# Kernel optimization log

Hardware: AMD Instinct MI355X
Metric: run time of the kernel (lower is better)

The kernel has to match this reference:

```python
import jax, jax.numpy as jnp
import numpy as np

CEP_ORDER = 255          # M
IR_LENGTH = 512          # N
BATCH = 131072
C_SCALE = 0.01           # keep the exponential-ish recurrence numerically tame


def setup_inputs() -> dict:
    key = jax.random.key(0)
    c = jax.random.normal(key, (BATCH, CEP_ORDER + 1), dtype=jnp.float32) * C_SCALE
    return {"c": c}


def _c2mpir(c, ir_length):
    # c: (..., M+1) -> h: (..., N)
    M = c.shape[-1] - 1
    ramp = jnp.arange(1, M + 1, dtype=c.dtype)
    h0 = jnp.exp(c[..., 0])                      # (...,)
    c1 = (c[..., 1:] * ramp)[..., ::-1]          # (..., M), flipped k*c_k
    # rolling buffer holds h[n-M .. n-1]; zeros stand in for negative indices,
    # which reproduces the truncated window h[max(0, n-M):n] of the original.
    buf0 = jnp.zeros_like(c1).at[..., -1].set(h0)
    ns = jnp.arange(1, ir_length, dtype=c.dtype)

    def step(buf, n):
        hn = jnp.einsum('...d,...d->...', buf, c1) / n      # (...,)
        buf = jnp.concatenate([buf[..., 1:], hn[..., None]], axis=-1)
        return buf, hn

    _, hs = jax.lax.scan(step, buf0, ns)         # (N-1, ...)
    h = jnp.concatenate([h0[None], hs], axis=0)  # (N, ...)
    return jnp.moveaxis(h, 0, -1)                # (..., N)


def reference(c):
    return _c2mpir(c, IR_LENGTH)
```

## Files before the change

### kernel.cpp

```cpp
#include <hip/hip_runtime.h>
#include <math.h>


constexpr int ROWS_PER_BLOCK = 32;
constexpr int THREADS = 256;
constexpr int CLEN = 256;
constexpr int NOUT = 512;
constexpr int RHALVES = 264;

typedef float f4 __attribute__((ext_vector_type(4)));
typedef _Float16 half2_t __attribute__((ext_vector_type(2)));

__device__ __forceinline__ float row8_sum(float v) {
  int x;
  x = __builtin_amdgcn_update_dpp(0, __float_as_int(v), 0xB1, 0xF, 0xF, true);
  v += __int_as_float(x);
  x = __builtin_amdgcn_update_dpp(0, __float_as_int(v), 0x4E, 0xF, 0xF, true);
  v += __int_as_float(x);
  x = __builtin_amdgcn_update_dpp(0, __float_as_int(v), 0x141, 0xF, 0xF, true);
  v += __int_as_float(x);
  return v;
}

#define DOTQ(P, wu, ub)                                                \
      { const half2_t q = __builtin_bit_cast(half2_t, (wu));           \
        A0 = __builtin_amdgcn_fdot2(q, P[(ub) + 7], A0, false);        \
        A1 = __builtin_amdgcn_fdot2(q, P[(ub) + 6], A1, false);        \
        A2 = __builtin_amdgcn_fdot2(q, P[(ub) + 5], A2, false);        \
        A3 = __builtin_amdgcn_fdot2(q, P[(ub) + 4], A3, false);        \
        A4 = __builtin_amdgcn_fdot2(q, P[(ub) + 3], A4, false);        \
        A5 = __builtin_amdgcn_fdot2(q, P[(ub) + 2], A5, false);        \
        A6 = __builtin_amdgcn_fdot2(q, P[(ub) + 1], A6, false);        \
        A7 = __builtin_amdgcn_fdot2(q, P[(ub) + 0], A7, false); }

#define ITER_TAIL(Y0EXPR)                                                \
      const float a0 = row8_sum(A0);                                     \
      const float a1 = row8_sum(A1);                                     \
      const float a2 = row8_sum(A2);                                     \
      const float a3 = row8_sum(A3);                                     \
      const float a4 = row8_sum(A4);                                     \
      const float a5 = row8_sum(A5);                                     \
      const float a6 = row8_sum(A6);                                     \
      const float a7 = row8_sum(A7);                                     \
      const int n = it * 8;                                              \
      const f4 ivA = *(const f4*)(&INV[n]);                              \
      const f4 ivB = *(const f4*)(&INV[n + 4]);                          \
      const float y0 = (Y0EXPR);                                         \
      const float y1 = fmaf(kc1, y0, a1) * ivA.y;                        \
      const float y2 = fmaf(kc1, y1, fmaf(kc2, y0, a2)) * ivA.z;         \
      const float y3 = fmaf(kc1, y2, fmaf(kc2, y1,                       \
                          fmaf(kc3, y0, a3))) * ivA.w;                   \
      const float y4 = fmaf(kc1, y3, fmaf(kc2, y2, fmaf(kc3, y1,         \
                          fmaf(kc4, y0, a4)))) * ivB.x;                  \
      const float y5 = fmaf(kc1, y4, fmaf(kc2, y3, fmaf(kc3, y2,         \
                          fmaf(kc4, y1, fmaf(kc5, y0, a5))))) * ivB.y;   \
      const float y6 = fmaf(kc1, y5, fmaf(kc2, y4, fmaf(kc3, y3,         \
                          fmaf(kc4, y2, fmaf(kc5, y1,                    \
                          fmaf(kc6, y0, a6)))))) * ivB.z;                \
      const float y7 = fmaf(kc1, y6, fmaf(kc2, y5, fmaf(kc3, y4,         \
                          fmaf(kc4, y3, fmaf(kc5, y2, fmaf(kc6, y1,      \
                          fmaf(kc7, y0, a7)))))))  * ivB.w;              \
      uint4 wq;                                                          \
      wq.x = __builtin_bit_cast(uint, __builtin_amdgcn_cvt_pkrtz(y0, y1)); \
      wq.y = __builtin_bit_cast(uint, __builtin_amdgcn_cvt_pkrtz(y2, y3)); \
      wq.z = __builtin_bit_cast(uint, __builtin_amdgcn_cvt_pkrtz(y4, y5)); \
      wq.w = __builtin_bit_cast(uint, __builtin_amdgcn_cvt_pkrtz(y6, y7)); \
      qn = wq;                                                           \
      wo = (wo + 16) & 508;                                              \
      if (s == 0) {                                                      \
        *(uint4*)(Hb + wo) = wq;      \
      }                                                                  \
      if ((it & 7) == s) {                                               \
        ys0 = y0; ys1 = y1; ys2 = y2; ys3 = y3;                          \
        ys4 = y4; ys5 = y5; ys6 = y6; ys7 = y7;                          \
      }                                                                  \
      if ((it & 7) == 7) {                                               \
        f4 v0; v0.x = ys0; v0.y = ys1; v0.z = ys2; v0.w = ys3;           \
        f4 v1; v1.x = ys4; v1.y = ys5; v1.z = ys6; v1.w = ys7;           \
        *(f4*)(gp) = v0;                                                 \
        *(f4*)(gp + 4) = v1;                                             \
        gp += 64;                                                        \
      }

__global__ __launch_bounds__(THREADS, 4) void cep2ir_kernel(
    const float* __restrict__ c, float* __restrict__ out, int nrows) {
  __shared__ ushort HF[ROWS_PER_BLOCK][RHALVES];
  __shared__ float INV[NOUT];

  const int tid = threadIdx.x;
  const int lane = tid & 63;
  const int wid = tid >> 6;
  const int s = lane & 7;
  const int rl = (wid << 3) | (lane >> 3);

  for (int i = tid; i < NOUT; i += THREADS)
    INV[i] = (i == 0) ? 0.0f : 1.0f / (float)i;
  uint* hz = (uint*)&HF[0][0];
  for (int i = tid; i < ROWS_PER_BLOCK * RHALVES / 2; i += THREADS)
    hz[i] = 0u;
  __syncthreads();

  const long long row = (long long)blockIdx.x * ROWS_PER_BLOCK + rl;
  if (row < nrows) {
    const float* __restrict__ crow = c + row * (long long)CLEN;

    const float kc1 = crow[1];
    const float kc2 = 2.0f * crow[2];
    const float kc3 = 3.0f * crow[3];
    const float kc4 = 4.0f * crow[4];
    const float kc5 = 5.0f * crow[5];
    const float kc6 = 6.0f * crow[6];
    const float kc7 = 7.0f * crow[7];
    const float h0val = expf(crow[0]);
    const bool is7 = (s == 7);

    char* __restrict__ Hb = (char*)&HF[rl][0];
    int wo = (-16) & 508;
    float* __restrict__ gp = out + row * (long long)NOUT + 8 * s;

    uint4 qn; qn.x = 0u; qn.y = 0u; qn.z = 0u; qn.w = 0u;

    float ys0 = 0.f, ys1 = 0.f, ys2 = 0.f, ys3 = 0.f;
    float ys4 = 0.f, ys5 = 0.f, ys6 = 0.f, ys7 = 0.f;

    {
      const int K1 = 128 - 16 * s;
      half2_t P1[22];
#pragma unroll
      for (int u = 0; u < 22; ++u) {
        const int kx = K1 + 7 - u;
        P1[u] = __builtin_bit_cast(half2_t, __builtin_amdgcn_cvt_pkrtz(
                    (float)kx * crow[kx], (float)(kx - 1) * crow[kx - 1]));
      }

#pragma unroll 2
      for (int it = 0; it < 16; ++it) {
        const int b0 = (16 * it + 256 + 32 * s) & 508;
        const int b1 = (b0 + 16) & 508;
        const uint4 u0 = *(const uint4*)(Hb + b0);
        const uint4 u1r = *(const uint4*)(Hb + b1);
        uint4 u1;
        u1.x = is7 ? qn.x : u1r.x;
        u1.y = is7 ? qn.y : u1r.y;
        u1.z = is7 ? qn.z : u1r.z;
        u1.w = is7 ? qn.w : u1r.w;

        float A0 = 0.f, A1 = 0.f, A2 = 0.f, A3 = 0.f;
        float A4 = 0.f, A5 = 0.f, A6 = 0.f, A7 = 0.f;
        DOTQ(P1, u0.x, 0)  DOTQ(P1, u0.y, 2)
        DOTQ(P1, u0.z, 4)  DOTQ(P1, u0.w, 6)
        DOTQ(P1, u1.x, 8)  DOTQ(P1, u1.y, 10)
        DOTQ(P1, u1.z, 12) DOTQ(P1, u1.w, 14)

        ITER_TAIL((it == 0) ? h0val : a0 * ivA.x)
      }
    }

    {
      const int K = 256 - 32 * s;
      half2_t P[38];
#pragma unroll
      for (int u = 0; u < 38; ++u) {
        const int kx = K + 7 - u;
        const int ky = kx - 1;
        const float px = (kx >= 1 && kx <= 255) ? (float)kx * crow[kx] : 0.0f;
        const float py = (ky >= 1 && ky <= 255) ? (float)ky * crow[ky] : 0.0f;
        P[u] = __builtin_bit_cast(half2_t, __builtin_amdgcn_cvt_pkrtz(px, py));
      }

      uint4 cw0 = *(const uint4*)(Hb + ((64 * s + 0  + 256) & 508));
      uint4 cw1 = *(const uint4*)(Hb + ((64 * s + 16 + 256) & 508));
      uint4 cw2 = *(const uint4*)(Hb + ((64 * s + 32 + 256) & 508));
      uint4 cw3 = *(const uint4*)(Hb + ((64 * s + 48 + 256) & 508));
      int ro0 = (64 * s + 0  + 272) & 508;
      int ro1 = (64 * s + 16 + 272) & 508;
      int ro2 = (64 * s + 32 + 272) & 508;
      int ro3 = (64 * s + 48 + 272) & 508;

#pragma unroll 2
      for (int it = 16; it < 64; ++it) {
        const uint4 pw0 = *(const uint4*)(Hb + ro0);
        const uint4 pw1 = *(const uint4*)(Hb + ro1);
        const uint4 pw2 = *(const uint4*)(Hb + ro2);
        const uint4 pw3 = *(const uint4*)(Hb + ro3);
        ro0 = (ro0 + 16) & 508; ro1 = (ro1 + 16) & 508;
        ro2 = (ro2 + 16) & 508; ro3 = (ro3 + 16) & 508;

        uint4 w3u;
        w3u.x = is7 ? qn.x : cw3.x;
        w3u.y = is7 ? qn.y : cw3.y;
        w3u.z = is7 ? qn.z : cw3.z;
        w3u.w = is7 ? qn.w : cw3.w;

        float A0 = 0.f, A1 = 0.f, A2 = 0.f, A3 = 0.f;
        float A4 = 0.f, A5 = 0.f, A6 = 0.f, A7 = 0.f;
        DOTQ(P, cw0.x, 0)  DOTQ(P, cw0.y, 2)
        DOTQ(P, cw0.z, 4)  DOTQ(P, cw0.w, 6)
        DOTQ(P, cw1.x, 8)  DOTQ(P, cw1.y, 10)
        DOTQ(P, cw1.z, 12) DOTQ(P, cw1.w, 14)
        DOTQ(P, cw2.x, 16) DOTQ(P, cw2.y, 18)
        DOTQ(P, cw2.z, 20) DOTQ(P, cw2.w, 22)
        DOTQ(P, w3u.x, 24) DOTQ(P, w3u.y, 26)
        DOTQ(P, w3u.z, 28) DOTQ(P, w3u.w, 30)

        ITER_TAIL(a0 * ivA.x)

        cw0 = pw0; cw1 = pw1; cw2 = pw2; cw3 = pw3;
      }
    }
  }
}

extern "C" void kernel_launch(void* const* d_in, const int* in_sizes, int n_in,
                              void* d_out, int out_size, void* d_ws, size_t ws_size,
                              hipStream_t stream) {
  const float* c = (const float*)d_in[0];
  float* out = (float*)d_out;
  const int nrows = in_sizes[0] / CLEN;
  const int nblocks = (nrows + ROWS_PER_BLOCK - 1) / ROWS_PER_BLOCK;
  hipLaunchKernelGGL(cep2ir_kernel, dim3(nblocks), dim3(THREADS), 0, stream,
                     c, out, nrows);
}
```

Baseline: 376.5 us.

## Add short-window first phase, swap DPP reductions for ds_swizzle, ping-pong phase-3 registers

Adds a new first phase covering the first eight output blocks, where only a small history window is nonzero, so those steps do 4 dot-product words instead of 8 and skip the second LDS read. Replaces the DPP row-reduction steps with ds_swizzle butterfly exchanges. Manually unrolls the main phase by two with ping-pong register sets, removing the per-iteration register copies. ds_swizzle goes through the LDS unit and has higher latency than DPP, which could lengthen the serial recurrence critical path.

```diff
diff --git a/kernel.cpp b/kernel.cpp
--- a/kernel.cpp
+++ b/kernel.cpp
@@ -13,11 +13,11 @@
 
 __device__ __forceinline__ float row8_sum(float v) {
   int x;
-  x = __builtin_amdgcn_update_dpp(0, __float_as_int(v), 0xB1, 0xF, 0xF, true);
+  x = __builtin_amdgcn_ds_swizzle(__float_as_int(v), 0x041F);
   v += __int_as_float(x);
-  x = __builtin_amdgcn_update_dpp(0, __float_as_int(v), 0x4E, 0xF, 0xF, true);
+  x = __builtin_amdgcn_ds_swizzle(__float_as_int(v), 0x081F);
   v += __int_as_float(x);
-  x = __builtin_amdgcn_update_dpp(0, __float_as_int(v), 0x141, 0xF, 0xF, true);
+  x = __builtin_amdgcn_ds_swizzle(__float_as_int(v), 0x101F);
   v += __int_as_float(x);
   return v;
 }
@@ -82,6 +82,32 @@
         gp += 64;                                                        \
       }
 
+#define P2_BODY(W0, W1, W2, W3, N0, N1, N2, N3)                          \
+    {                                                                    \
+      N0 = *(const uint4*)(Hb + ro0);                                    \
+      N1 = *(const uint4*)(Hb + ro1);                                    \
+      N2 = *(const uint4*)(Hb + ro2);                                    \
+      N3 = *(const uint4*)(Hb + ro3);                                    \
+      ro0 = (ro0 + 16) & 508; ro1 = (ro1 + 16) & 508;                    \
+      ro2 = (ro2 + 16) & 508; ro3 = (ro3 + 16) & 508;                    \
+      uint4 w3u;                                                         \
+      w3u.x = is7 ? qn.x : W3.x;                                         \
+      w3u.y = is7 ? qn.y : W3.y;                                         \
+      w3u.z = is7 ? qn.z : W3.z;                                         \
+      w3u.w = is7 ? qn.w : W3.w;                                         \
+      float A0 = 0.f, A1 = 0.f, A2 = 0.f, A3 = 0.f;                      \
+      float A4 = 0.f, A5 = 0.f, A6 = 0.f, A7 = 0.f;                      \
+      DOTQ(P, W0.x, 0)   DOTQ(P, W0.y, 2)                                \
+      DOTQ(P, W0.z, 4)   DOTQ(P, W0.w, 6)                                \
+      DOTQ(P, W1.x, 8)   DOTQ(P, W1.y, 10)                               \
+      DOTQ(P, W1.z, 12)  DOTQ(P, W1.w, 14)                               \
+      DOTQ(P, W2.x, 16)  DOTQ(P, W2.y, 18)                               \
+      DOTQ(P, W2.z, 20)  DOTQ(P, W2.w, 22)                               \
+      DOTQ(P, w3u.x, 24) DOTQ(P, w3u.y, 26)                              \
+      DOTQ(P, w3u.z, 28) DOTQ(P, w3u.w, 30)                              \
+      ITER_TAIL(a0 * ivA.x)                                              \
+    }
+
 __global__ __launch_bounds__(THREADS, 4) void cep2ir_kernel(
     const float* __restrict__ c, float* __restrict__ out, int nrows) {
   __shared__ ushort HF[ROWS_PER_BLOCK][RHALVES];
@@ -124,6 +150,34 @@
     float ys4 = 0.f, ys5 = 0.f, ys6 = 0.f, ys7 = 0.f;
 
     {
+      const int K0 = 64 - 8 * s;
+      half2_t P0[14];
+#pragma unroll
+      for (int u = 0; u < 14; ++u) {
+        const int kx = K0 + 7 - u;
+        P0[u] = __builtin_bit_cast(half2_t, __builtin_amdgcn_cvt_pkrtz(
+                    (float)kx * crow[kx], (float)(kx - 1) * crow[kx - 1]));
+      }
+#pragma unroll 2
+      for (int it = 0; it < 8; ++it) {
+        const int b = (16 * it + 384 + 16 * s) & 508;
+        const uint4 r0 = *(const uint4*)(Hb + b);
+        uint4 u0;
+        u0.x = is7 ? qn.x : r0.x;
+        u0.y = is7 ? qn.y : r0.y;
+        u0.z = is7 ? qn.z : r0.z;
+        u0.w = is7 ? qn.w : r0.w;
+
+        float A0 = 0.f, A1 = 0.f, A2 = 0.f, A3 = 0.f;
+        float A4 = 0.f, A5 = 0.f, A6 = 0.f, A7 = 0.f;
+        DOTQ(P0, u0.x, 0) DOTQ(P0, u0.y, 2)
+        DOTQ(P0, u0.z, 4) DOTQ(P0, u0.w, 6)
+
+        ITER_TAIL((it == 0) ? h0val : a0 * ivA.x)
+      }
+    }
+
+    {
       const int K1 = 128 - 16 * s;
       half2_t P1[22];
 #pragma unroll
@@ -132,9 +186,8 @@
         P1[u] = __builtin_bit_cast(half2_t, __builtin_amdgcn_cvt_pkrtz(
                     (float)kx * crow[kx], (float)(kx - 1) * crow[kx - 1]));
       }
-
 #pragma unroll 2
-      for (int it = 0; it < 16; ++it) {
+      for (int it = 8; it < 16; ++it) {
         const int b0 = (16 * it + 256 + 32 * s) & 508;
         const int b1 = (b0 + 16) & 508;
         const uint4 u0 = *(const uint4*)(Hb + b0);
@@ -152,7 +205,7 @@
         DOTQ(P1, u1.x, 8)  DOTQ(P1, u1.y, 10)
         DOTQ(P1, u1.z, 12) DOTQ(P1, u1.w, 14)
 
-        ITER_TAIL((it == 0) ? h0val : a0 * ivA.x)
+        ITER_TAIL(a0 * ivA.x)
       }
     }
 
@@ -176,36 +229,13 @@
       int ro1 = (64 * s + 16 + 272) & 508;
       int ro2 = (64 * s + 32 + 272) & 508;
       int ro3 = (64 * s + 48 + 272) & 508;
-
-#pragma unroll 2
-      for (int it = 16; it < 64; ++it) {
-        const uint4 pw0 = *(const uint4*)(Hb + ro0);
-        const uint4 pw1 = *(const uint4*)(Hb + ro1);
-        const uint4 pw2 = *(const uint4*)(Hb + ro2);
-        const uint4 pw3 = *(const uint4*)(Hb + ro3);
-        ro0 = (ro0 + 16) & 508; ro1 = (ro1 + 16) & 508;
-        ro2 = (ro2 + 16) & 508; ro3 = (ro3 + 16) & 508;
-
-        uint4 w3u;
-        w3u.x = is7 ? qn.x : cw3.x;
-        w3u.y = is7 ? qn.y : cw3.y;
-        w3u.z = is7 ? qn.z : cw3.z;
-        w3u.w = is7 ? qn.w : cw3.w;
-
-        float A0 = 0.f, A1 = 0.f, A2 = 0.f, A3 = 0.f;
-        float A4 = 0.f, A5 = 0.f, A6 = 0.f, A7 = 0.f;
-        DOTQ(P, cw0.x, 0)  DOTQ(P, cw0.y, 2)
-        DOTQ(P, cw0.z, 4)  DOTQ(P, cw0.w, 6)
-        DOTQ(P, cw1.x, 8)  DOTQ(P, cw1.y, 10)
-        DOTQ(P, cw1.z, 12) DOTQ(P, cw1.w, 14)
-        DOTQ(P, cw2.x, 16) DOTQ(P, cw2.y, 18)
-        DOTQ(P, cw2.z, 20) DOTQ(P, cw2.w, 22)
-        DOTQ(P, w3u.x, 24) DOTQ(P, w3u.y, 26)
-        DOTQ(P, w3u.z, 28) DOTQ(P, w3u.w, 30)
-
-        ITER_TAIL(a0 * ivA.x)
-
-        cw0 = pw0; cw1 = pw1; cw2 = pw2; cw3 = pw3;
+      uint4 pw0, pw1, pw2, pw3;
+
+      for (int itp = 16; itp < 64; itp += 2) {
+        { const int it = itp;
+          P2_BODY(cw0, cw1, cw2, cw3, pw0, pw1, pw2, pw3) }
+        { const int it = itp + 1;
+          P2_BODY(pw0, pw1, pw2, pw3, cw0, cw1, cw2, cw3) }
       }
     }
   }
```

After: 401.8 us. 1.07x slower.
